# Optimization experiments

Measured on AMD Instinct MI355X. Metric: run time of the kernel, lower is better.

Reference implementation:

```python
import jax, jax.numpy as jnp
import numpy as np

BS, N_AGGR, D, OUT = 4096, 4, 128, 128  # d_in per child; T is (A, D+1, D+1, OUT)


def setup_inputs() -> dict:
    key = jax.random.key(0)
    k0, k1, k2 = jax.random.split(key, 3)
    x0 = jax.random.normal(k0, (BS, N_AGGR, D), dtype=jnp.float32)
    x1 = jax.random.normal(k1, (BS, N_AGGR, D), dtype=jnp.float32)
    # xavier-uniform-style init for each T_j, stacked over the aggregator axis
    fan_in = (D + 1) * (D + 1) * OUT // (D + 1)  # torch fan heuristic scale; exact init not load-bearing
    bound = float(np.sqrt(6.0 / ((D + 1) + (D + 1) * OUT)))
    T = jax.random.uniform(k2, (N_AGGR, D + 1, D + 1, OUT), dtype=jnp.float32,
                           minval=-bound, maxval=bound)
    return {"x0": x0, "x1": x1, "T": T}


def reference(x0, x1, T):
    # x0, x1: (bs, A, D); T: (A, D+1, D+1, OUT)
    bs, A, _ = x0.shape
    ones = jnp.ones((bs, A, 1), dtype=x0.dtype)
    h0 = jnp.concatenate([x0, ones], axis=2)            # (bs, A, D+1)
    # first contraction (the per-head matmul loop, fused): (bs, A, D+1, OUT)
    r = jnp.einsum('bai,aijo->bajo', h0, T)
    h1 = jnp.concatenate([x1, ones], axis=2)            # (bs, A, D+1)
    # second contraction (the per-head bmm loop, fused): (bs, A, OUT)
    out = jnp.einsum('baj,bajo->bao', h1, r)
    return out
```

## Files before the change

### kernel.cpp

```cpp
#include <hip/hip_runtime.h>
#include <stdint.h>
#include <stddef.h>

#define NA     4
#define DDIM   128
#define OUTD   128
#define BM     128
#define BN     128
#define NTILES 261
#define TILE_B 16384
#define OUT_ELEMS (4096 * NA * OUTD)

typedef _Float16 f16;
typedef __attribute__((ext_vector_type(8)))  _Float16 f16x8;
typedef __attribute__((ext_vector_type(4)))  float    f32x4;

static const size_t TB_BYTES = (size_t)NA * NTILES * TILE_B;
static const size_t WS2 = TB_BYTES + (size_t)2 * OUT_ELEMS * 4;

__global__ __launch_bounds__(256) void prep_kernel(const float* __restrict__ T,
                                                   f16* __restrict__ Tb) {
    int blk  = blockIdx.x;
    int a    = blk / NTILES;
    int tile = blk - a * NTILES;
    int t    = threadIdx.x;
    f16* base = Tb + (size_t)blk * (TILE_B / 2);
    #pragma unroll
    for (int u = 0; u < 4; ++u) {
        int v   = t + u * 256;
        int w   = v >> 7;
        int col = v & 127;
        f16x8 ov;
        #pragma unroll
        for (int e = 0; e < 8; ++e) {
            int k = tile * 64 + w * 8 + e;
            int i = -1, j = 0;
            if (k < 16384)       { i = k & 127;   j = k >> 7;    }
            else if (k < 16512)  { i = 128;       j = k - 16384; }
            else if (k < 16640)  { i = k - 16512; j = 128;       }
            else if (k == 16640) { i = 128;       j = 128;       }
            float val = 0.f;
            if (i >= 0) val = T[(((size_t)a * 129 + i) * 129 + j) * 128 + col];
            ov[e] = (f16)val;
        }
        *(f16x8*)(base + (size_t)v * 8) = ov;
    }
}

__device__ __forceinline__ f16x8 pack_f16x8(f32x4 a, f32x4 b) {
    f16x8 h;
    #pragma unroll
    for (int e = 0; e < 4; ++e) { h[e] = (f16)a[e]; h[e + 4] = (f16)b[e]; }
    return h;
}

template <bool ATOMIC>
__global__ __launch_bounds__(512, 2) void gemm_kernel(const float* __restrict__ x0,
                                                      const float* __restrict__ x1,
                                                      const f16* __restrict__ Tb,
                                                      float* __restrict__ dst) {
    __shared__ __align__(16) f16 h1t[64 * 128];

    int bid = blockIdx.x;
    int pr  = bid & 7;
    int mt  = bid >> 3;
    int a   = pr >> 1;
    int ks  = pr & 1;

    int t    = threadIdx.x;
    int lane = t & 63, wid = t >> 6;
    int wm   = wid >> 2, wn = wid & 3;
    int l15  = lane & 15, g = lane >> 4;
    int b0   = mt * BM;

    const char* tbb = (const char*)Tb + (size_t)a * NTILES * TILE_B;

    {
        int row = t & 127, part = t >> 7;
        const float* x1r = x1 + ((size_t)(b0 + row) * NA + a) * DDIM + ks * 64 + part * 16;
        #pragma unroll
        for (int q = 0; q < 4; ++q) {
            f32x4 v = *(const f32x4*)(x1r + q * 4);
            #pragma unroll
            for (int e = 0; e < 4; ++e)
                h1t[(part * 16 + q * 4 + e) * 128 + row] = (f16)v[e];
        }
    }
    f16x8 h0r[4][2][2];
    #pragma unroll
    for (int mf = 0; mf < 4; ++mf) {
        int row = b0 + wm * 64 + mf * 16 + l15;
        const float* x0r = x0 + ((size_t)row * NA + a) * DDIM;
        #pragma unroll
        for (int par = 0; par < 2; ++par)
            #pragma unroll
            for (int s = 0; s < 2; ++s) {
                int ib = par * 64 + s * 32 + g * 8;
                h0r[mf][par][s] = pack_f16x8(*(const f32x4*)(x0r + ib),
                                             *(const f32x4*)(x0r + ib + 4));
            }
    }
    __syncthreads();

    const char* bp = tbb + (size_t)(ks * 128) * TILE_B + ((size_t)g * 128 + wn * 32 + l15) * 16;
    #define BFOFF(nf, s) ((s) * 8192 + (nf) * 256)

    f16x8 bA[4], bB[4];
    #pragma unroll
    for (int nf = 0; nf < 2; ++nf)
        #pragma unroll
        for (int s = 0; s < 2; ++s) {
            bA[nf * 2 + s] = *(const f16x8*)(bp + BFOFF(nf, s));
            bB[nf * 2 + s] = *(const f16x8*)(bp + TILE_B + BFOFF(nf, s));
        }

    f32x4 acc[4][2];
    #pragma unroll
    for (int mf = 0; mf < 4; ++mf)
        #pragma unroll
        for (int nf = 0; nf < 2; ++nf) acc[mf][nf] = (f32x4)0.f;

    #pragma unroll 1
    for (int p = 0; p < 64; ++p) {
        f16 h1v[4];
        #pragma unroll
        for (int mf = 0; mf < 4; ++mf)
            h1v[mf] = h1t[p * 128 + wm * 64 + mf * 16 + l15];

        f16x8 af0[4][2], af1[4][2];
        #pragma unroll
        for (int mf = 0; mf < 4; ++mf)
            #pragma unroll
            for (int s = 0; s < 2; ++s) {
                af0[mf][s] = h0r[mf][0][s] * h1v[mf];
                af1[mf][s] = h0r[mf][1][s] * h1v[mf];
            }

        #pragma unroll
        for (int s = 0; s < 2; ++s)
            #pragma unroll
            for (int nf = 0; nf < 2; ++nf)
                #pragma unroll
                for (int mf = 0; mf < 4; ++mf)
                    acc[mf][nf] = __builtin_amdgcn_mfma_f32_16x16x32_f16(
                        af0[mf][s], bA[nf * 2 + s], acc[mf][nf], 0, 0, 0);
        {
            int nxt = 2 * p + 2; if (nxt > 127) nxt = 127;
            const char* q = bp + (size_t)nxt * TILE_B;
            #pragma unroll
            for (int nf = 0; nf < 2; ++nf)
                #pragma unroll
                for (int s = 0; s < 2; ++s)
                    bA[nf * 2 + s] = *(const f16x8*)(q + BFOFF(nf, s));
        }
        #pragma unroll
        for (int s = 0; s < 2; ++s)
            #pragma unroll
            for (int nf = 0; nf < 2; ++nf)
                #pragma unroll
                for (int mf = 0; mf < 4; ++mf)
                    acc[mf][nf] = __builtin_amdgcn_mfma_f32_16x16x32_f16(
                        af1[mf][s], bB[nf * 2 + s], acc[mf][nf], 0, 0, 0);
        {
            int nxt = 2 * p + 3; if (nxt > 127) nxt = 127;
            const char* q = bp + (size_t)nxt * TILE_B;
            #pragma unroll
            for (int nf = 0; nf < 2; ++nf)
                #pragma unroll
                for (int s = 0; s < 2; ++s)
                    bB[nf * 2 + s] = *(const f16x8*)(q + BFOFF(nf, s));
        }
    }

    int ncorr = (ks == 0) ? 2 : 3;
    for (int tt = 0; tt < ncorr; ++tt) {
        int tile = (ks == 0) ? ((tt == 0) ? 256 : 258)
                             : ((tt == 0) ? 257 : (tt == 1) ? 259 : 260);
        const char* q = tbb + (size_t)tile * TILE_B + ((size_t)g * 128 + wn * 32 + l15) * 16;
        f16x8 bt[4];
        #pragma unroll
        for (int nf = 0; nf < 2; ++nf)
            #pragma unroll
            for (int s = 0; s < 2; ++s)
                bt[nf * 2 + s] = *(const f16x8*)(q + BFOFF(nf, s));

        #pragma unroll
        for (int s = 0; s < 2; ++s)
            #pragma unroll
            for (int mf = 0; mf < 4; ++mf) {
                int row = wm * 64 + mf * 16 + l15;
                f16x8 af;
                if (tile == 256 || tile == 257) {
                    #pragma unroll
                    for (int e = 0; e < 8; ++e)
                        af[e] = h1t[(s * 32 + g * 8 + e) * 128 + row];
                } else if (tile == 258) {
                    af = h0r[mf][0][s];
                } else if (tile == 259) {
                    af = h0r[mf][1][s];
                } else {
                    af = (f16x8)(f16)0.f;
                    if (s == 0 && g == 0) af[0] = (f16)1.f;
                }
                #pragma unroll
                for (int nf = 0; nf < 2; ++nf)
                    acc[mf][nf] = __builtin_amdgcn_mfma_f32_16x16x32_f16(
                        af, bt[nf * 2 + s], acc[mf][nf], 0, 0, 0);
            }
    }

    float* base = ATOMIC ? dst : dst + (size_t)ks * OUT_ELEMS;
    #pragma unroll
    for (int mf = 0; mf < 4; ++mf)
        #pragma unroll
        for (int nf = 0; nf < 2; ++nf)
            #pragma unroll
            for (int r = 0; r < 4; ++r) {
                int orow = b0 + wm * 64 + mf * 16 + g * 4 + r;
                int ocol = wn * 32 + nf * 16 + l15;
                size_t off = ((size_t)orow * NA + a) * OUTD + ocol;
                if (ATOMIC) unsafeAtomicAdd(&base[off], acc[mf][nf][r]);
                else        base[off] = acc[mf][nf][r];
            }
    #undef BFOFF
}

__global__ __launch_bounds__(256) void reduce_kernel(const float* __restrict__ P,
                                                     float* __restrict__ out) {
    int i = blockIdx.x * 256 + threadIdx.x;
    f32x4 s = ((const f32x4*)P)[i];
    s += ((const f32x4*)(P + OUT_ELEMS))[i];
    ((f32x4*)out)[i] = s;
}

__global__ __launch_bounds__(128) void fallback_kernel(const float* __restrict__ x0,
                                                       const float* __restrict__ x1,
                                                       const float* __restrict__ T,
                                                       float* __restrict__ out) {
    int ba = blockIdx.x;
    int b = ba >> 2, a = ba & 3;
    int o = threadIdx.x;
    const float* h0 = x0 + ((size_t)b * NA + a) * DDIM;
    const float* h1 = x1 + ((size_t)b * NA + a) * DDIM;
    float acc = 0.f;
    for (int i = 0; i < 129; ++i) {
        float h0i = (i < 128) ? h0[i] : 1.f;
        const float* Trow = T + (((size_t)a * 129 + i) * 129) * 128 + o;
        float part = 0.f;
        for (int j = 0; j < 129; ++j) {
            float h1j = (j < 128) ? h1[j] : 1.f;
            part += h1j * Trow[(size_t)j * 128];
        }
        acc += h0i * part;
    }
    out[((size_t)b * NA + a) * OUTD + o] = acc;
}

extern "C" void kernel_launch(void* const* d_in, const int* in_sizes, int n_in,
                              void* d_out, int out_size, void* d_ws, size_t ws_size,
                              hipStream_t stream) {
    const float* x0 = (const float*)d_in[0];
    const float* x1 = (const float*)d_in[1];
    const float* T  = (const float*)d_in[2];
    float* out = (float*)d_out;

    if (ws_size < TB_BYTES) {
        fallback_kernel<<<4096 * NA, 128, 0, stream>>>(x0, x1, T, out);
        return;
    }

    f16* Tb = (f16*)d_ws;
    prep_kernel<<<NA * NTILES, 256, 0, stream>>>(T, Tb);

    if (ws_size >= WS2) {
        float* P = (float*)((char*)d_ws + TB_BYTES);
        gemm_kernel<false><<<256, 512, 0, stream>>>(x0, x1, Tb, P);
        reduce_kernel<<<OUT_ELEMS / 4 / 256, 256, 0, stream>>>(P, out);
    } else {
        hipMemsetAsync(d_out, 0, (size_t)out_size * sizeof(float), stream);
        gemm_kernel<true><<<256, 512, 0, stream>>>(x0, x1, Tb, out);
    }
}
```

Baseline: 96.54 us.

## Split K dimension four ways and remap blocks to XCDs

Raises the split-K factor from two to four, so 512 blocks each handle 32 j-pairs instead of 64, with per-XCD block remapping so each XCD works on a fixed (aggregator, k-split) pair for weight cache locality. The correction tiles are redistributed across the four splits, and the reduce kernel now sums four partial buffers. Launch bounds ask for 4 blocks per CU. This fills more of the GPU and improves L2 reuse, at the cost of more partial-output traffic, a larger reduction, and a larger workspace requirement.

Result: slower. 200.4 us (+107.6%).

```diff
diff --git a/kernel.cpp b/kernel.cpp
--- a/kernel.cpp
+++ b/kernel.cpp
@@ -10,13 +10,14 @@
 #define NTILES 261
 #define TILE_B 16384
 #define OUT_ELEMS (4096 * NA * OUTD)
+#define NKS    4
 
 typedef _Float16 f16;
 typedef __attribute__((ext_vector_type(8)))  _Float16 f16x8;
 typedef __attribute__((ext_vector_type(4)))  float    f32x4;
 
 static const size_t TB_BYTES = (size_t)NA * NTILES * TILE_B;
-static const size_t WS2 = TB_BYTES + (size_t)2 * OUT_ELEMS * 4;
+static const size_t WS_NEED  = TB_BYTES + (size_t)NKS * OUT_ELEMS * 4;
 
 __global__ __launch_bounds__(256) void prep_kernel(const float* __restrict__ T,
                                                    f16* __restrict__ Tb) {
@@ -55,17 +56,18 @@
 }
 
 template <bool ATOMIC>
-__global__ __launch_bounds__(512, 2) void gemm_kernel(const float* __restrict__ x0,
+__global__ __launch_bounds__(512, 4) void gemm_kernel(const float* __restrict__ x0,
                                                       const float* __restrict__ x1,
                                                       const f16* __restrict__ Tb,
                                                       float* __restrict__ dst) {
-    __shared__ __align__(16) f16 h1t[64 * 128];
+    __shared__ __align__(16) f16 h1t[128 * 128];
 
     int bid = blockIdx.x;
-    int pr  = bid & 7;
-    int mt  = bid >> 3;
-    int a   = pr >> 1;
-    int ks  = pr & 1;
+    int xcd = bid & 7, idx = bid >> 3;
+    int pair = xcd * 2 + (idx >> 5);
+    int mt  = idx & 31;
+    int a   = pair & 3;
+    int ks  = pair >> 2;
 
     int t    = threadIdx.x;
     int lane = t & 63, wid = t >> 6;
@@ -77,13 +79,13 @@
 
     {
         int row = t & 127, part = t >> 7;
-        const float* x1r = x1 + ((size_t)(b0 + row) * NA + a) * DDIM + ks * 64 + part * 16;
-        #pragma unroll
-        for (int q = 0; q < 4; ++q) {
+        const float* x1r = x1 + ((size_t)(b0 + row) * NA + a) * DDIM + part * 32;
+        #pragma unroll
+        for (int q = 0; q < 8; ++q) {
             f32x4 v = *(const f32x4*)(x1r + q * 4);
             #pragma unroll
             for (int e = 0; e < 4; ++e)
-                h1t[(part * 16 + q * 4 + e) * 128 + row] = (f16)v[e];
+                h1t[(part * 32 + q * 4 + e) * 128 + row] = (f16)v[e];
         }
     }
     f16x8 h0r[4][2][2];
@@ -102,7 +104,7 @@
     }
     __syncthreads();
 
-    const char* bp = tbb + (size_t)(ks * 128) * TILE_B + ((size_t)g * 128 + wn * 32 + l15) * 16;
+    const char* bp = tbb + (size_t)(ks * 64) * TILE_B + ((size_t)g * 128 + wn * 32 + l15) * 16;
     #define BFOFF(nf, s) ((s) * 8192 + (nf) * 256)
 
     f16x8 bA[4], bB[4];
@@ -121,11 +123,12 @@
         for (int nf = 0; nf < 2; ++nf) acc[mf][nf] = (f32x4)0.f;
 
     #pragma unroll 1
-    for (int p = 0; p < 64; ++p) {
+    for (int p = 0; p < 32; ++p) {
+        int jg = ks * 32 + p;
         f16 h1v[4];
         #pragma unroll
         for (int mf = 0; mf < 4; ++mf)
-            h1v[mf] = h1t[p * 128 + wm * 64 + mf * 16 + l15];
+            h1v[mf] = h1t[jg * 128 + wm * 64 + mf * 16 + l15];
 
         f16x8 af0[4][2], af1[4][2];
         #pragma unroll
@@ -145,7 +148,7 @@
                     acc[mf][nf] = __builtin_amdgcn_mfma_f32_16x16x32_f16(
                         af0[mf][s], bA[nf * 2 + s], acc[mf][nf], 0, 0, 0);
         {
-            int nxt = 2 * p + 2; if (nxt > 127) nxt = 127;
+            int nxt = 2 * p + 2; if (nxt > 63) nxt = 63;
             const char* q = bp + (size_t)nxt * TILE_B;
             #pragma unroll
             for (int nf = 0; nf < 2; ++nf)
@@ -162,7 +165,7 @@
                     acc[mf][nf] = __builtin_amdgcn_mfma_f32_16x16x32_f16(
                         af1[mf][s], bB[nf * 2 + s], acc[mf][nf], 0, 0, 0);
         {
-            int nxt = 2 * p + 3; if (nxt > 127) nxt = 127;
+            int nxt = 2 * p + 3; if (nxt > 63) nxt = 63;
             const char* q = bp + (size_t)nxt * TILE_B;
             #pragma unroll
             for (int nf = 0; nf < 2; ++nf)
@@ -172,10 +175,13 @@
         }
     }
 
-    int ncorr = (ks == 0) ? 2 : 3;
+    int ncorr = (ks == 2) ? 2 : 1;
     for (int tt = 0; tt < ncorr; ++tt) {
-        int tile = (ks == 0) ? ((tt == 0) ? 256 : 258)
-                             : ((tt == 0) ? 257 : (tt == 1) ? 259 : 260);
+        int tile;
+        if      (ks == 0) tile = 256;
+        else if (ks == 1) tile = 257;
+        else if (ks == 2) tile = (tt == 0) ? 258 : 260;
+        else              tile = 259;
         const char* q = tbb + (size_t)tile * TILE_B + ((size_t)g * 128 + wn * 32 + l15) * 16;
         f16x8 bt[4];
         #pragma unroll
@@ -191,9 +197,10 @@
                 int row = wm * 64 + mf * 16 + l15;
                 f16x8 af;
                 if (tile == 256 || tile == 257) {
+                    int cb = (tile == 257) ? 64 : 0;
                     #pragma unroll
                     for (int e = 0; e < 8; ++e)
-                        af[e] = h1t[(s * 32 + g * 8 + e) * 128 + row];
+                        af[e] = h1t[(cb + s * 32 + g * 8 + e) * 128 + row];
                 } else if (tile == 258) {
                     af = h0r[mf][0][s];
                 } else if (tile == 259) {
@@ -229,7 +236,9 @@
                                                      float* __restrict__ out) {
     int i = blockIdx.x * 256 + threadIdx.x;
     f32x4 s = ((const f32x4*)P)[i];
-    s += ((const f32x4*)(P + OUT_ELEMS))[i];
+    #pragma unroll
+    for (int k = 1; k < NKS; ++k)
+        s += ((const f32x4*)(P + (size_t)k * OUT_ELEMS))[i];
     ((f32x4*)out)[i] = s;
 }
 
@@ -272,12 +281,12 @@
     f16* Tb = (f16*)d_ws;
     prep_kernel<<<NA * NTILES, 256, 0, stream>>>(T, Tb);
 
-    if (ws_size >= WS2) {
+    if (ws_size >= WS_NEED) {
         float* P = (float*)((char*)d_ws + TB_BYTES);
-        gemm_kernel<false><<<256, 512, 0, stream>>>(x0, x1, Tb, P);
+        gemm_kernel<false><<<512, 512, 0, stream>>>(x0, x1, Tb, P);
         reduce_kernel<<<OUT_ELEMS / 4 / 256, 256, 0, stream>>>(P, out);
     } else {
         hipMemsetAsync(d_out, 0, (size_t)out_size * sizeof(float), stream);
-        gemm_kernel<true><<<256, 512, 0, stream>>>(x0, x1, Tb, out);
-    }
-}
+        gemm_kernel<true><<<512, 512, 0, stream>>>(x0, x1, Tb, out);
+    }
+}
```
